# Kernel optimization log

Measured on AMD Instinct MI355X. Metric: run time of the kernel, lower is better.

Reference implementation:

```python
import jax, jax.numpy as jnp
import numpy as np
import math

K = 7
B, C, H, W = 16, 3, 256, 256
N = 50000
ANGLE = 30.0; TRANS = 0.45; SHEAR = 0.3; SCALE0, SCALE1 = 1.0, 0.5  # self.scale assumed [1.0,0.5] (upstream AutoDO)


def _bilinear(img, xs, ys):
    # img: (C,Hs,Ws); xs,ys: (Ho,Wo) pixel coords; border padding (clamp)
    Cc, Hs, Ws = img.shape
    xs = jnp.clip(xs, 0.0, Ws - 1.0)
    ys = jnp.clip(ys, 0.0, Hs - 1.0)
    x0 = jnp.floor(xs); y0 = jnp.floor(ys)
    wx = xs - x0; wy = ys - y0
    x0i = x0.astype(jnp.int32); y0i = y0.astype(jnp.int32)
    x1i = jnp.minimum(x0i + 1, Ws - 1); y1i = jnp.minimum(y0i + 1, Hs - 1)
    Ia = img[:, y0i, x0i]; Ib = img[:, y0i, x1i]
    Ic = img[:, y1i, x0i]; Id = img[:, y1i, x1i]
    return Ia * (1 - wx) * (1 - wy) + Ib * wx * (1 - wy) + Ic * (1 - wx) * wy + Id * wx * wy


def _resize(x, Ho, Wo):
    # torch F.interpolate bilinear, align_corners=False, no antialias
    Bb, Cc, Hs, Ws = x.shape
    ys = (jnp.arange(Ho, dtype=x.dtype) + 0.5) * (Hs / Ho) - 0.5
    xs = (jnp.arange(Wo, dtype=x.dtype) + 0.5) * (Ws / Wo) - 0.5
    Y, X = jnp.meshgrid(ys, xs, indexing='ij')
    return jax.vmap(lambda im: _bilinear(im, X, Y))(x)


def _warp_perspective(x, M, Ho, Wo):
    # kornia.warp_perspective: dst(p) = src(M^-1 p), bilinear, border padding, align_corners=True
    Bb, Cc, Hs, Ws = x.shape
    Minv = jnp.linalg.inv(M)  # (B,3,3)
    yy, xx = jnp.meshgrid(jnp.arange(Ho, dtype=x.dtype), jnp.arange(Wo, dtype=x.dtype), indexing='ij')
    pts = jnp.stack([xx.ravel(), yy.ravel(), jnp.ones(Ho * Wo, dtype=x.dtype)])  # (3, Ho*Wo)
    src = jnp.einsum('bij,jn->bin', Minv, pts)
    xs = (src[:, 0] / src[:, 2]).reshape(Bb, Ho, Wo)
    ys = (src[:, 1] / src[:, 2]).reshape(Bb, Ho, Wo)
    return jax.vmap(_bilinear)(x, xs, ys)


def _forward(x, paramP, paramM, gumbel_u, eps, idx):
    dt = x.dtype
    pP = jax.nn.sigmoid(paramP[:, idx])  # (K,B)
    logits = jnp.stack([jnp.log(pP).ravel(), jnp.log(1.0 - pP).ravel()], axis=1)  # (K*B,2)
    g = -jnp.log(-jnp.log(gumbel_u))
    y_soft = jax.nn.softmax(logits + g, axis=1)  # tau=1
    y_hard = jax.nn.one_hot(jnp.argmax(y_soft, axis=1), 2, dtype=y_soft.dtype)
    y = y_hard + y_soft - jax.lax.stop_gradient(y_soft)  # straight-through hard gumbel
    sP = y[:, 0].reshape(K, B)
    sM = jax.nn.sigmoid(paramM[:, idx]) * eps  # (K,B)
    ang = sP[0] * sM[0] * ANGLE
    # replicate torch's cat(W//2 * ones(B), H//2 * ones(B)).view(-1,2) layout exactly
    ctr = jnp.concatenate([jnp.full((B,), W // 2, dt), jnp.full((B,), H // 2, dt)]).reshape(-1, 2)
    sx = SCALE0 + sP[5] * sM[5] * SCALE1
    sy = SCALE0 + sP[6] * sM[6] * SCALE1
    rad = jnp.deg2rad(ang); ca = jnp.cos(rad); sa = jnp.sin(rad)
    # kornia get_rotation_matrix2d: rot=[[c,s],[-s,c]] @ diag(sx,sy); t = ctr - rot@ctr
    sr = jnp.stack([jnp.stack([ca * sx, sa * sy], -1), jnp.stack([-sa * sx, ca * sy], -1)], -2)  # (B,2,2)
    t = ctr - jnp.einsum('bij,bj->bi', sr, ctr)
    eye = jnp.broadcast_to(jnp.eye(3, dtype=dt), (B, 3, 3))
    R = eye.at[:, :2, :2].set(sr).at[:, :2, 2].set(t)
    T = eye.at[:, 0, 2].set(W * sP[1] * sM[1] * TRANS).at[:, 1, 2].set(H * sP[2] * sM[2] * TRANS)
    S = eye.at[:, 0, 1].set(sP[3] * sM[3] * SHEAR).at[:, 1, 0].set(sP[4] * sM[4] * SHEAR)
    M = S @ T @ R
    x_up = _resize(x, 4 * H, 4 * W)
    x_w = _warp_perspective(x_up, M, 4 * H, 4 * W)
    return _resize(x_w, H, W)


def setup_inputs() -> dict:
    key = jax.random.key(0)
    k1, k2, k3, k4 = jax.random.split(key, 4)
    p = 1.0 / (K - 2)
    prob_logit = math.log(p / (1.0 - p))
    m = 5.0 / 10.0
    magn_logit = math.log(m / (1.0 - m))
    return {
        'x': jax.random.uniform(k1, (B, C, H, W), jnp.float32),
        'paramP': jnp.full((K, N), prob_logit, jnp.float32),
        'paramM': jnp.full((K, N), magn_logit, jnp.float32),
        'gumbel_u': jax.random.uniform(k2, (K * B, 2), jnp.float32, minval=1e-6, maxval=1.0 - 1e-6),
        'eps': jax.random.normal(k3, (K, B), jnp.float32),
        'idx': jax.random.randint(k4, (B,), 0, N, jnp.int32),
    }


def reference(x, paramP, paramM, gumbel_u, eps, idx):
    return _forward(x, paramP, paramM, gumbel_u, eps, idx)
```

## Files before the change

### kernel.cpp

```cpp
#include <hip/hip_runtime.h>
#include <math.h>


__global__ __launch_bounds__(64) void compute_minv(
    const float* __restrict__ paramP, const float* __restrict__ paramM,
    const float* __restrict__ gumbel_u, const float* __restrict__ eps,
    const int* __restrict__ idx, float* __restrict__ minv, int N)
{
    int b = threadIdx.x;
    if (b >= 16) return;
    int id = idx[b];
    float sP[7], sM[7];
#pragma unroll
    for (int k = 0; k < 7; ++k) {
        float vP = paramP[k * N + id];
        float pP = 1.0f / (1.0f + expf(-vP));
        float l0 = logf(pP);
        float l1 = logf(1.0f - pP);
        float u0 = gumbel_u[(k * 16 + b) * 2 + 0];
        float u1 = gumbel_u[(k * 16 + b) * 2 + 1];
        float g0 = -logf(-logf(u0));
        float g1 = -logf(-logf(u1));
        sP[k] = (l0 + g0 >= l1 + g1) ? 1.0f : 0.0f;
        float vM = paramM[k * N + id];
        float sig = 1.0f / (1.0f + expf(-vM));
        sM[k] = sig * eps[k * 16 + b];
    }
    float ang = sP[0] * sM[0] * 30.0f;
    float rad = ang * 0.017453292519943295f;
    float ca = cosf(rad), sa = sinf(rad);
    float sx = 1.0f + sP[5] * sM[5] * 0.5f;
    float sy = 1.0f + sP[6] * sM[6] * 0.5f;
    float sr00 = ca * sx, sr01 = sa * sy;
    float sr10 = -sa * sx, sr11 = ca * sy;
    float t0 = 128.0f - (sr00 + sr01) * 128.0f;
    float t1 = 128.0f - (sr10 + sr11) * 128.0f;
    float tx = 256.0f * sP[1] * sM[1] * 0.45f;
    float ty = 256.0f * sP[2] * sM[2] * 0.45f;
    float sh01 = sP[3] * sM[3] * 0.3f;
    float sh10 = sP[4] * sM[4] * 0.3f;
    float e0 = t0 + tx, e1 = t1 + ty;
    float a  = sr00 + sh01 * sr10;
    float bb = sr01 + sh01 * sr11;
    float txm = e0 + sh01 * e1;
    float c  = sh10 * sr00 + sr10;
    float d  = sh10 * sr01 + sr11;
    float tym = sh10 * e0 + e1;
    float det = a * d - bb * c;
    float rdet = 1.0f / det;
    float* o = minv + b * 8;
    o[0] = d * rdet;
    o[1] = -bb * rdet;
    o[2] = (bb * tym - d * txm) * rdet;
    o[3] = -c * rdet;
    o[4] = a * rdet;
    o[5] = (c * txm - a * tym) * rdet;
}

struct Up { int i0; float w; };

__device__ __forceinline__ Up upc(int v) {
    float u = fmaf(0.25f, (float)v, -0.375f);
    u = fminf(fmaxf(u, 0.0f), 255.0f);
    float f = floorf(u);
    Up r; r.i0 = (int)f; r.w = u - f;
    return r;
}

__global__ __launch_bounds__(256) void fused_warp(
    const float* __restrict__ x, const float* __restrict__ minv,
    float* __restrict__ out)
{
    int j = blockIdx.x * 16 + threadIdx.x;
    int i = blockIdx.y * 16 + threadIdx.y;
    int b = blockIdx.z;
    const float* mi = minv + b * 8;
    float m00 = mi[0], m01 = mi[1], m02 = mi[2];
    float m10 = mi[3], m11 = mi[4], m12 = mi[5];
    const float* xb = x + b * 3 * 65536;
    float acc0 = 0.0f, acc1 = 0.0f, acc2 = 0.0f;
#pragma unroll
    for (int s = 0; s < 4; ++s) {
        float X = (float)(4 * j + 1 + (s & 1));
        float Y = (float)(4 * i + 1 + (s >> 1));
        float xs = fmaf(m00, X, fmaf(m01, Y, m02));
        float ys = fmaf(m10, X, fmaf(m11, Y, m12));
        xs = fminf(fmaxf(xs, 0.0f), 1023.0f);
        ys = fminf(fmaxf(ys, 0.0f), 1023.0f);
        float fx = floorf(xs), fy = floorf(ys);
        float wx = xs - fx, wy = ys - fy;
        int x0 = (int)fx, y0 = (int)fy;
        int x1 = min(x0 + 1, 1023), y1 = min(y0 + 1, 1023);
        Up cx0 = upc(x0), cx1 = upc(x1);
        Up ry0 = upc(y0), ry1 = upc(y1);
        float A0 = 1.0f - wx, A1 = wx;
        float cb0 = A1 * (1.0f - cx1.w), cb1 = A1 * cx1.w;
        bool dc = (cx1.i0 != cx0.i0);
        float cw0 = A0 * (1.0f - cx0.w) + (dc ? 0.0f : cb0);
        float cw1 = A0 * cx0.w + (dc ? cb0 : cb1);
        float cw2 = dc ? cb1 : 0.0f;
        float B0 = 1.0f - wy, B1 = wy;
        float rb0 = B1 * (1.0f - ry1.w), rb1 = B1 * ry1.w;
        bool dr = (ry1.i0 != ry0.i0);
        float rw0 = B0 * (1.0f - ry0.w) + (dr ? 0.0f : rb0);
        float rw1 = B0 * ry0.w + (dr ? rb0 : rb1);
        float rw2 = dr ? rb1 : 0.0f;
        int cb = cx0.i0, rb = ry0.i0;
        int c0i = cb, c1i = min(cb + 1, 255), c2i = min(cb + 2, 255);
        int ro0 = rb * 256;
        int ro1 = min(rb + 1, 255) * 256;
        int ro2 = min(rb + 2, 255) * 256;
        {
            const float* p = xb;
            float t0 = fmaf(cw2, p[ro0 + c2i], fmaf(cw1, p[ro0 + c1i], cw0 * p[ro0 + c0i]));
            float t1 = fmaf(cw2, p[ro1 + c2i], fmaf(cw1, p[ro1 + c1i], cw0 * p[ro1 + c0i]));
            float t2 = fmaf(cw2, p[ro2 + c2i], fmaf(cw1, p[ro2 + c1i], cw0 * p[ro2 + c0i]));
            acc0 += fmaf(rw2, t2, fmaf(rw1, t1, rw0 * t0));
        }
        {
            const float* p = xb + 65536;
            float t0 = fmaf(cw2, p[ro0 + c2i], fmaf(cw1, p[ro0 + c1i], cw0 * p[ro0 + c0i]));
            float t1 = fmaf(cw2, p[ro1 + c2i], fmaf(cw1, p[ro1 + c1i], cw0 * p[ro1 + c0i]));
            float t2 = fmaf(cw2, p[ro2 + c2i], fmaf(cw1, p[ro2 + c1i], cw0 * p[ro2 + c0i]));
            acc1 += fmaf(rw2, t2, fmaf(rw1, t1, rw0 * t0));
        }
        {
            const float* p = xb + 131072;
            float t0 = fmaf(cw2, p[ro0 + c2i], fmaf(cw1, p[ro0 + c1i], cw0 * p[ro0 + c0i]));
            float t1 = fmaf(cw2, p[ro1 + c2i], fmaf(cw1, p[ro1 + c1i], cw0 * p[ro1 + c0i]));
            float t2 = fmaf(cw2, p[ro2 + c2i], fmaf(cw1, p[ro2 + c1i], cw0 * p[ro2 + c0i]));
            acc2 += fmaf(rw2, t2, fmaf(rw1, t1, rw0 * t0));
        }
    }
    int obase = ((b * 3) * 256 + i) * 256 + j;
    out[obase]          = 0.25f * acc0;
    out[obase + 65536]  = 0.25f * acc1;
    out[obase + 131072] = 0.25f * acc2;
}

extern "C" void kernel_launch(void* const* d_in, const int* in_sizes, int n_in,
                              void* d_out, int out_size, void* d_ws, size_t ws_size,
                              hipStream_t stream) {
    const float* x      = (const float*)d_in[0];
    const float* paramP = (const float*)d_in[1];
    const float* paramM = (const float*)d_in[2];
    const float* gumbel = (const float*)d_in[3];
    const float* eps    = (const float*)d_in[4];
    const int*   idx    = (const int*)d_in[5];
    float* out  = (float*)d_out;
    float* minv = (float*)d_ws;
    int N = in_sizes[1] / 7;

    hipLaunchKernelGGL(compute_minv, dim3(1), dim3(64), 0, stream,
                       paramP, paramM, gumbel, eps, idx, minv, N);
    hipLaunchKernelGGL(fused_warp, dim3(16, 16, 16), dim3(16, 16, 1), 0, stream,
                       x, minv, out);
}
```

Measured before the change: 98.47 us.

## Merge horizontally adjacent subsamples into a 4x4 footprint read with float4 loads

The warp kernel now handles the four supersamples per output pixel as two pairs of horizontally adjacent samples. For each pair it builds combined 4x4 separable weights over a shared source footprint, and each channel reads that footprint with four unaligned float4 row loads instead of many scalar gathers. Column bases near the right edge are clamped and the weights shifted to match. This cuts gather instructions and address arithmetic, at the cost of extra weight math and registers. It assumes the pair's footprint always fits in 4x4 source pixels, which could break under large scale or shear magnitudes.

```diff
diff --git a/kernel.cpp b/kernel.cpp
--- a/kernel.cpp
+++ b/kernel.cpp
@@ -1,6 +1,14 @@
 #include <hip/hip_runtime.h>
 #include <math.h>
 
+
+typedef float floatx4 __attribute__((ext_vector_type(4)));
+
+__device__ __forceinline__ floatx4 load4(const float* p) {
+    floatx4 v;
+    __builtin_memcpy(&v, p, sizeof(v));
+    return v;
+}
 
 __global__ __launch_bounds__(64) void compute_minv(
     const float* __restrict__ paramP, const float* __restrict__ paramM,
@@ -67,6 +75,25 @@
     return r;
 }
 
+struct Trip { float w0, w1, w2; int base; };
+
+__device__ __forceinline__ Trip merged3(float s) {
+    float f = floorf(s);
+    float fr = s - f;
+    int v0 = (int)f;
+    int v1 = min(v0 + 1, 1023);
+    Up c0 = upc(v0), c1 = upc(v1);
+    float A0 = 1.0f - fr, A1 = fr;
+    float b0 = A1 * (1.0f - c1.w), b1 = A1 * c1.w;
+    bool d = (c1.i0 != c0.i0);
+    Trip t;
+    t.w0 = A0 * (1.0f - c0.w) + (d ? 0.0f : b0);
+    t.w1 = A0 * c0.w + (d ? b0 : b1);
+    t.w2 = d ? b1 : 0.0f;
+    t.base = c0.i0;
+    return t;
+}
+
 __global__ __launch_bounds__(256) void fused_warp(
     const float* __restrict__ x, const float* __restrict__ minv,
     float* __restrict__ out)
@@ -78,64 +105,92 @@
     float m00 = mi[0], m01 = mi[1], m02 = mi[2];
     float m10 = mi[3], m11 = mi[4], m12 = mi[5];
     const float* xb = x + b * 3 * 65536;
-    float acc0 = 0.0f, acc1 = 0.0f, acc2 = 0.0f;
-#pragma unroll
-    for (int s = 0; s < 4; ++s) {
-        float X = (float)(4 * j + 1 + (s & 1));
-        float Y = (float)(4 * i + 1 + (s >> 1));
-        float xs = fmaf(m00, X, fmaf(m01, Y, m02));
-        float ys = fmaf(m10, X, fmaf(m11, Y, m12));
-        xs = fminf(fmaxf(xs, 0.0f), 1023.0f);
-        ys = fminf(fmaxf(ys, 0.0f), 1023.0f);
-        float fx = floorf(xs), fy = floorf(ys);
-        float wx = xs - fx, wy = ys - fy;
-        int x0 = (int)fx, y0 = (int)fy;
-        int x1 = min(x0 + 1, 1023), y1 = min(y0 + 1, 1023);
-        Up cx0 = upc(x0), cx1 = upc(x1);
-        Up ry0 = upc(y0), ry1 = upc(y1);
-        float A0 = 1.0f - wx, A1 = wx;
-        float cb0 = A1 * (1.0f - cx1.w), cb1 = A1 * cx1.w;
-        bool dc = (cx1.i0 != cx0.i0);
-        float cw0 = A0 * (1.0f - cx0.w) + (dc ? 0.0f : cb0);
-        float cw1 = A0 * cx0.w + (dc ? cb0 : cb1);
-        float cw2 = dc ? cb1 : 0.0f;
-        float B0 = 1.0f - wy, B1 = wy;
-        float rb0 = B1 * (1.0f - ry1.w), rb1 = B1 * ry1.w;
-        bool dr = (ry1.i0 != ry0.i0);
-        float rw0 = B0 * (1.0f - ry0.w) + (dr ? 0.0f : rb0);
-        float rw1 = B0 * ry0.w + (dr ? rb0 : rb1);
-        float rw2 = dr ? rb1 : 0.0f;
-        int cb = cx0.i0, rb = ry0.i0;
-        int c0i = cb, c1i = min(cb + 1, 255), c2i = min(cb + 2, 255);
-        int ro0 = rb * 256;
-        int ro1 = min(rb + 1, 255) * 256;
-        int ro2 = min(rb + 2, 255) * 256;
-        {
-            const float* p = xb;
-            float t0 = fmaf(cw2, p[ro0 + c2i], fmaf(cw1, p[ro0 + c1i], cw0 * p[ro0 + c0i]));
-            float t1 = fmaf(cw2, p[ro1 + c2i], fmaf(cw1, p[ro1 + c1i], cw0 * p[ro1 + c0i]));
-            float t2 = fmaf(cw2, p[ro2 + c2i], fmaf(cw1, p[ro2 + c1i], cw0 * p[ro2 + c0i]));
-            acc0 += fmaf(rw2, t2, fmaf(rw1, t1, rw0 * t0));
+    float acc[3] = {0.f, 0.f, 0.f};
+
+#pragma unroll
+    for (int p = 0; p < 2; ++p) {
+        float XA = (float)(4 * j + 1);
+        float Yp = (float)(4 * i + 1 + p);
+        float xAu = fmaf(m00, XA, fmaf(m01, Yp, m02));
+        float yAu = fmaf(m10, XA, fmaf(m11, Yp, m12));
+        float xBu = xAu + m00;
+        float yBu = yAu + m10;
+        float xsA = fminf(fmaxf(xAu, 0.f), 1023.f);
+        float ysA = fminf(fmaxf(yAu, 0.f), 1023.f);
+        float xsB = fminf(fmaxf(xBu, 0.f), 1023.f);
+        float ysB = fminf(fmaxf(yBu, 0.f), 1023.f);
+        Trip cA = merged3(xsA), cB = merged3(xsB);
+        Trip rA = merged3(ysA), rB = merged3(ysB);
+        int cb = min(cA.base, cB.base);
+        int rb = min(rA.base, rB.base);
+        float CA[4], CB[4], RA[4], RB[4];
+        bool sa_ = (cA.base != cb);
+        CA[0] = sa_ ? 0.f : cA.w0;
+        CA[1] = sa_ ? cA.w0 : cA.w1;
+        CA[2] = sa_ ? cA.w1 : cA.w2;
+        CA[3] = sa_ ? cA.w2 : 0.f;
+        bool sb_ = (cB.base != cb);
+        CB[0] = sb_ ? 0.f : cB.w0;
+        CB[1] = sb_ ? cB.w0 : cB.w1;
+        CB[2] = sb_ ? cB.w1 : cB.w2;
+        CB[3] = sb_ ? cB.w2 : 0.f;
+        bool ra_ = (rA.base != rb);
+        RA[0] = ra_ ? 0.f : rA.w0;
+        RA[1] = ra_ ? rA.w0 : rA.w1;
+        RA[2] = ra_ ? rA.w1 : rA.w2;
+        RA[3] = ra_ ? rA.w2 : 0.f;
+        bool rb_ = (rB.base != rb);
+        RB[0] = rb_ ? 0.f : rB.w0;
+        RB[1] = rb_ ? rB.w0 : rB.w1;
+        RB[2] = rb_ ? rB.w1 : rB.w2;
+        RB[3] = rb_ ? rB.w2 : 0.f;
+
+        float W[4][4];
+#pragma unroll
+        for (int r = 0; r < 4; ++r)
+#pragma unroll
+            for (int c = 0; c < 4; ++c)
+                W[r][c] = fmaf(RB[r], CB[c], RA[r] * CA[c]);
+
+        int base = cb;
+        if (cb > 252) {
+            int shift = cb - 252;
+            base = 252;
+            for (int s = 0; s < shift; ++s) {
+#pragma unroll
+                for (int r = 0; r < 4; ++r) {
+                    W[r][3] = W[r][2];
+                    W[r][2] = W[r][1];
+                    W[r][1] = W[r][0];
+                    W[r][0] = 0.f;
+                }
+            }
         }
-        {
-            const float* p = xb + 65536;
-            float t0 = fmaf(cw2, p[ro0 + c2i], fmaf(cw1, p[ro0 + c1i], cw0 * p[ro0 + c0i]));
-            float t1 = fmaf(cw2, p[ro1 + c2i], fmaf(cw1, p[ro1 + c1i], cw0 * p[ro1 + c0i]));
-            float t2 = fmaf(cw2, p[ro2 + c2i], fmaf(cw1, p[ro2 + c1i], cw0 * p[ro2 + c0i]));
-            acc1 += fmaf(rw2, t2, fmaf(rw1, t1, rw0 * t0));
-        }
-        {
-            const float* p = xb + 131072;
-            float t0 = fmaf(cw2, p[ro0 + c2i], fmaf(cw1, p[ro0 + c1i], cw0 * p[ro0 + c0i]));
-            float t1 = fmaf(cw2, p[ro1 + c2i], fmaf(cw1, p[ro1 + c1i], cw0 * p[ro1 + c0i]));
-            float t2 = fmaf(cw2, p[ro2 + c2i], fmaf(cw1, p[ro2 + c1i], cw0 * p[ro2 + c0i]));
-            acc2 += fmaf(rw2, t2, fmaf(rw1, t1, rw0 * t0));
+
+        int e0 = rb * 256 + base;
+        int e1 = min(rb + 1, 255) * 256 + base;
+        int e2 = min(rb + 2, 255) * 256 + base;
+        int e3 = min(rb + 3, 255) * 256 + base;
+
+#pragma unroll
+        for (int ch = 0; ch < 3; ++ch) {
+            const float* pc = xb + ch * 65536;
+            floatx4 L0 = load4(pc + e0);
+            floatx4 L1 = load4(pc + e1);
+            floatx4 L2 = load4(pc + e2);
+            floatx4 L3 = load4(pc + e3);
+            float s0 = fmaf(W[0][3], L0.w, fmaf(W[0][2], L0.z, fmaf(W[0][1], L0.y, W[0][0] * L0.x)));
+            float s1 = fmaf(W[1][3], L1.w, fmaf(W[1][2], L1.z, fmaf(W[1][1], L1.y, W[1][0] * L1.x)));
+            float s2 = fmaf(W[2][3], L2.w, fmaf(W[2][2], L2.z, fmaf(W[2][1], L2.y, W[2][0] * L2.x)));
+            float s3 = fmaf(W[3][3], L3.w, fmaf(W[3][2], L3.z, fmaf(W[3][1], L3.y, W[3][0] * L3.x)));
+            acc[ch] += (s0 + s1) + (s2 + s3);
         }
     }
+
     int obase = ((b * 3) * 256 + i) * 256 + j;
-    out[obase]          = 0.25f * acc0;
-    out[obase + 65536]  = 0.25f * acc1;
-    out[obase + 131072] = 0.25f * acc2;
+    out[obase]          = 0.25f * acc[0];
+    out[obase + 65536]  = 0.25f * acc[1];
+    out[obase + 131072] = 0.25f * acc[2];
 }
 
 extern "C" void kernel_launch(void* const* d_in, const int* in_sizes, int n_in,
```

Measured after the change: 89.11 us. -9.5%, faster.
